# Kernel optimization log

Hardware: AMD Instinct MI355X
Metric: run time of the kernel (lower is better)

## Reference

```python
import jax, jax.numpy as jnp
import numpy as np

# dims: batch N, queries Q, frames F, patches-per-frame L, heads H, head_dim D
N, Q, F, L, H, D = 32, 64, 16, 196, 12, 64
E = H * D          # embed_dim = 768
K = F * L          # kv length = 3136


def setup_inputs() -> dict:
    key = jax.random.key(0)
    kq, kk, kv, km, kw1, kw2 = jax.random.split(key, 6)
    q = jax.random.normal(kq, (N, Q, E), dtype=jnp.float32)
    k = jax.random.normal(kk, (N, K, H, D), dtype=jnp.float32)
    v = jax.random.normal(kv, (N, K, H, D), dtype=jnp.float32)
    # frame-padding mask; guarantee >=1 valid patch per frame so the
    # per-frame softmax never sees an all -inf group (NaN otherwise)
    m = jax.random.bernoulli(km, 0.9, (N, K))
    m = m.reshape(N, F, L).at[:, :, 0].set(True).reshape(N, K)
    W_in = jax.random.normal(kw1, (E, E), dtype=jnp.float32) * 0.02   # in_proj (n_act=1)
    W_out = jax.random.normal(kw2, (E, E), dtype=jnp.float32) * 0.02  # out_proj
    return {"q": q, "k": k, "v": v, "m": m, "W_in": W_in, "W_out": W_out}


def reference(q, k, v, m, W_in, W_out):
    n, nq, e = q.shape
    h, d = H, e // H
    # in_proj (no bias) then split into heads; n_act == 1 so qs has one element
    qs = (q @ W_in.T).reshape(n, nq, h, d)
    # scaled QK affinity: [n, Q, K, h]
    aff = jnp.einsum('nqhc,nkhc->nqkh', qs * (d ** -0.5), k)
    # frame mask broadcast over queries and heads
    aff = jnp.where(m[:, None, :, None], aff, -jnp.inf)
    kn = aff.shape[2]
    # grouped softmax over patches within each frame (dim=-2 of the view)
    aff = jax.nn.softmax(aff.reshape(n, nq, F, kn // F, h), axis=-2)
    aff = aff.reshape(n, nq, kn, h)
    # mix with v and output projection
    mix = jnp.einsum('nqlh,nlhc->nqhc', aff, v)
    out = mix.reshape(n, nq, e) @ W_out.T
    # second return: stacked flattened qs, shape [n, n_act=1, Q, E]
    qs_out = qs.reshape(n, nq, e)[:, None]
    return out, qs_out
```

## Files before the change

kernel.cpp:

```cpp
#include <hip/hip_runtime.h>
#include <hip/hip_bf16.h>
#include <cfloat>

#define N_B 32
#define QN 64
#define FN 16
#define LP 196
#define HN 12
#define DH 64
#define EE 768
#define KLEN 3136
#define FPB 2
#define KROWS 208
#define VST 256

typedef short s16x4 __attribute__((ext_vector_type(4)));
typedef __bf16 bf16x4 __attribute__((ext_vector_type(4)));
typedef __bf16 bf16x8 __attribute__((ext_vector_type(8)));
typedef float f32x4 __attribute__((ext_vector_type(4)));
typedef unsigned u32x2 __attribute__((ext_vector_type(2)));

__device__ __forceinline__ bf16x8 cvt8(f32x4 a, f32x4 b) {
    bf16x8 r;
    r[0] = (__bf16)a[0]; r[1] = (__bf16)a[1]; r[2] = (__bf16)a[2]; r[3] = (__bf16)a[3];
    r[4] = (__bf16)b[0]; r[5] = (__bf16)b[1]; r[6] = (__bf16)b[2]; r[7] = (__bf16)b[3];
    return r;
}
__device__ __forceinline__ unsigned short bfb(float x) {
    return __builtin_bit_cast(unsigned short, (__bf16)x);
}
__device__ __forceinline__ unsigned pkbf(float lo, float hi) {
    return (unsigned)bfb(lo) | ((unsigned)bfb(hi) << 16);
}

__device__ __forceinline__ f32x4 mfma16(s16x4 a, s16x4 b, f32x4 c) {
#if __has_builtin(__builtin_amdgcn_mfma_f32_16x16x16_bf16)
    return __builtin_amdgcn_mfma_f32_16x16x16_bf16(__builtin_bit_cast(bf16x4, a),
                                                   __builtin_bit_cast(bf16x4, b), c, 0, 0, 0);
#elif __has_builtin(__builtin_amdgcn_mfma_f32_16x16x16bf16_1k)
    return __builtin_amdgcn_mfma_f32_16x16x16bf16_1k(a, b, c, 0, 0, 0);
#else
    f32x4 d;
    asm volatile("v_mfma_f32_16x16x16_bf16 %0, %1, %2, %3"
                 : "=v"(d) : "v"(a), "v"(b), "v"(c));
    return d;
#endif
}

__global__ __launch_bounds__(256) void gemm_mfma(const float* __restrict__ A,
                                                 const float* __restrict__ W,
                                                 float* __restrict__ C) {
    __shared__ unsigned short As[64 * 72];
    __shared__ unsigned short Ws[48 * 72];
    const int t = threadIdx.x;
    const int w = t >> 6, lane = t & 63, lr = lane & 15, lg = lane >> 4;
    const int m0 = blockIdx.x * 64;
    const int n0 = blockIdx.y * 48;

    f32x4 acc[3];
#pragma unroll
    for (int ct = 0; ct < 3; ++ct) acc[ct] = (f32x4){0.f, 0.f, 0.f, 0.f};

    for (int k0 = 0; k0 < EE; k0 += 32) {
        {
            int row = t >> 2, cb = t & 3;
            const float* src = A + (size_t)(m0 + row) * EE + k0 + cb * 8;
            f32x4 a = *(const f32x4*)src, b = *(const f32x4*)(src + 4);
            *(bf16x8*)&As[row * 72 + cb * 8] = cvt8(a, b);
        }
        if (t < 192) {
            int row = t >> 2, cb = t & 3;
            const float* src = W + (size_t)(n0 + row) * EE + k0 + cb * 8;
            f32x4 a = *(const f32x4*)src, b = *(const f32x4*)(src + 4);
            *(bf16x8*)&Ws[row * 72 + cb * 8] = cvt8(a, b);
        }
        __syncthreads();
        bf16x8 a = *(const bf16x8*)&As[(w * 16 + lr) * 72 + lg * 8];
#pragma unroll
        for (int ct = 0; ct < 3; ++ct) {
            bf16x8 b = *(const bf16x8*)&Ws[(ct * 16 + lr) * 72 + lg * 8];
            acc[ct] = __builtin_amdgcn_mfma_f32_16x16x32_bf16(a, b, acc[ct], 0, 0, 0);
        }
        __syncthreads();
    }
#pragma unroll
    for (int ct = 0; ct < 3; ++ct)
#pragma unroll
        for (int r = 0; r < 4; ++r)
            C[(size_t)(m0 + w * 16 + lg * 4 + r) * EE + n0 + ct * 16 + lr] = acc[ct][r];
}

__global__ __launch_bounds__(256) void zero_f32(float* __restrict__ p, int n4) {
    int i = blockIdx.x * 256 + threadIdx.x;
    if (i < n4) ((float4*)p)[i] = make_float4(0.f, 0.f, 0.f, 0.f);
}

__global__ __launch_bounds__(256, 2) void attn_mfma(const float* __restrict__ qs_g,
                                                    const float* __restrict__ k_g,
                                                    const float* __restrict__ v_g,
                                                    const int* __restrict__ m_g,
                                                    float* __restrict__ mix_g) {
    const int h = blockIdx.x, fg = blockIdx.y, n = blockIdx.z;

    __shared__ __attribute__((aligned(16))) unsigned short KV_s[64 * VST];
    __shared__ __attribute__((aligned(16))) float bias_s[224];

    const int t = threadIdx.x;
    const int w = t >> 6, lane = t & 63, lr = lane & 15, lg = lane >> 4;

    bf16x8 qb0, qb1;
    {
        const float* qp = qs_g + ((size_t)n * QN + w * 16 + lr) * EE + h * DH + lg * 8;
        f32x4 a = *(const f32x4*)qp, b = *(const f32x4*)(qp + 4);
        f32x4 c = *(const f32x4*)(qp + 32), d = *(const f32x4*)(qp + 36);
#pragma unroll
        for (int i = 0; i < 4; ++i) { a[i] *= 0.125f; b[i] *= 0.125f; c[i] *= 0.125f; d[i] *= 0.125f; }
        qb0 = cvt8(a, b);
        qb1 = cvt8(c, d);
    }

    float mix[4][4];
#pragma unroll
    for (int dt = 0; dt < 4; ++dt)
#pragma unroll
        for (int r = 0; r < 4; ++r) mix[dt][r] = 0.f;

    for (int ff = 0; ff < FPB; ++ff) {
        const size_t kbase = (size_t)n * KLEN + (size_t)(fg * FPB + ff) * LP;

        __syncthreads();

#pragma unroll
        for (int u = 0; u < 7; ++u) {
            int unit = t + 256 * u;
            if (unit < KROWS * 8) {
                int p = unit >> 3, blk = unit & 7;
                f32x4 a = {0.f, 0.f, 0.f, 0.f}, b = {0.f, 0.f, 0.f, 0.f};
                if (p < LP) {
                    const float* src = k_g + ((kbase + p) * HN + h) * DH + blk * 8;
                    a = *(const f32x4*)src;
                    b = *(const f32x4*)(src + 4);
                }
                *(bf16x8*)&KV_s[p * 64 + ((blk ^ (p & 7)) << 3)] = cvt8(a, b);
            }
        }
        if (t < 224) {
            float bv = -1e30f;
            if (t < LP && m_g[kbase + t] != 0) bv = 0.f;
            bias_s[t] = bv;
        }
        __syncthreads();

        f32x4 sc[13];
        __builtin_amdgcn_s_setprio(1);
#pragma unroll
        for (int tl = 0; tl < 13; ++tl) {
            int row = tl * 16 + lr;
            bf16x8 a0 = *(const bf16x8*)&KV_s[row * 64 + ((lg ^ (lr & 7)) << 3)];
            bf16x8 a1 = *(const bf16x8*)&KV_s[row * 64 + (((4 + lg) ^ (lr & 7)) << 3)];
            f32x4 z = {0.f, 0.f, 0.f, 0.f};
            z = __builtin_amdgcn_mfma_f32_16x16x32_bf16(a0, qb0, z, 0, 0, 0);
            sc[tl] = __builtin_amdgcn_mfma_f32_16x16x32_bf16(a1, qb1, z, 0, 0, 0);
        }
        __builtin_amdgcn_s_setprio(0);

        f32x4 va[4], vb[4];
#pragma unroll
        for (int u = 0; u < 4; ++u) {
            int unit = t + 256 * u;
            int pp = unit >> 3, d4 = unit & 7;
            int p0 = pp * 2;
            va[u] = (f32x4){0.f, 0.f, 0.f, 0.f};
            vb[u] = (f32x4){0.f, 0.f, 0.f, 0.f};
            if (p0 < LP) {
                const float* vg = v_g + ((kbase + p0) * HN + h) * DH + d4 * 4;
                va[u] = *(const f32x4*)vg;
                if (p0 + 1 < LP) vb[u] = *(const f32x4*)(vg + (size_t)HN * DH);
            }
        }

        float mx = -FLT_MAX;
#pragma unroll
        for (int tl = 0; tl < 13; ++tl) {
            f32x4 bv = *(const f32x4*)&bias_s[tl * 16 + lg * 4];
#pragma unroll
            for (int r = 0; r < 4; ++r) {
                float sv = sc[tl][r] + bv[r];
                sc[tl][r] = sv;
                mx = fmaxf(mx, sv);
            }
        }
        mx = fmaxf(mx, __shfl_xor(mx, 16));
        mx = fmaxf(mx, __shfl_xor(mx, 32));
        float sum = 0.f;
#pragma unroll
        for (int tl = 0; tl < 13; ++tl) {
            float e0 = __expf(sc[tl][0] - mx);
            float e1 = __expf(sc[tl][1] - mx);
            float e2 = __expf(sc[tl][2] - mx);
            float e3 = __expf(sc[tl][3] - mx);
            sum += (e0 + e1) + (e2 + e3);
            sc[tl][0] = e0; sc[tl][1] = e1; sc[tl][2] = e2; sc[tl][3] = e3;
        }
        sum += __shfl_xor(sum, 16);
        sum += __shfl_xor(sum, 32);
        float inv = 1.0f / sum;
        unsigned pk[13][2];
#pragma unroll
        for (int tl = 0; tl < 13; ++tl) {
            pk[tl][0] = pkbf(sc[tl][0] * inv, sc[tl][1] * inv);
            pk[tl][1] = pkbf(sc[tl][2] * inv, sc[tl][3] * inv);
        }

        __syncthreads();

#pragma unroll
        for (int u = 0; u < 4; ++u) {
            int unit = t + 256 * u;
            int pp = unit >> 3, d4 = unit & 7;
            int p0 = pp * 2;
            if (p0 < KROWS) {
                int blk = p0 >> 3, sub = p0 & 7;
#pragma unroll
                for (int i = 0; i < 4; ++i) {
                    int row = d4 * 4 + i;
                    int g = (row + 2 * (row >> 2)) & 7;
                    *(unsigned*)&KV_s[row * VST + (((blk ^ g) << 3) | sub)] = pkbf(va[u][i], vb[u][i]);
                }
            }
        }
#pragma unroll
        for (int u = 0; u < 4; ++u) {
            int unit = t + 256 * u;
            int pp = unit >> 3, d4 = unit & 7;
            int p0 = pp * 2;
            va[u] = (f32x4){0.f, 0.f, 0.f, 0.f};
            vb[u] = (f32x4){0.f, 0.f, 0.f, 0.f};
            if (p0 < LP) {
                const float* vg = v_g + ((kbase + p0) * HN + h) * DH + (8 + d4) * 4;
                va[u] = *(const f32x4*)vg;
                if (p0 + 1 < LP) vb[u] = *(const f32x4*)(vg + (size_t)HN * DH);
            }
        }
        __syncthreads();

        __builtin_amdgcn_s_setprio(1);
#pragma unroll
        for (int dt = 0; dt < 2; ++dt) {
            int row = dt * 16 + lr;
            int g = (row + 2 * (row >> 2)) & 7;
            f32x4 acc = {mix[dt][0], mix[dt][1], mix[dt][2], mix[dt][3]};
#pragma unroll
            for (int kt = 0; kt < 13; ++kt) {
                int c0 = kt * 16 + lg * 4;
                s16x4 b = *(const s16x4*)&KV_s[row * VST + ((((c0 >> 3) ^ g) << 3) | (c0 & 7))];
                s16x4 a = __builtin_bit_cast(s16x4, (u32x2){pk[kt][0], pk[kt][1]});
                acc = mfma16(a, b, acc);
            }
#pragma unroll
            for (int r = 0; r < 4; ++r) mix[dt][r] = acc[r];
        }
        __builtin_amdgcn_s_setprio(0);

#pragma unroll
        for (int u = 0; u < 4; ++u) {
            int unit = t + 256 * u;
            int pp = unit >> 3, d4 = unit & 7;
            int p0 = pp * 2;
            if (p0 < KROWS) {
                int blk = p0 >> 3, sub = p0 & 7;
#pragma unroll
                for (int i = 0; i < 4; ++i) {
                    int row = 32 + d4 * 4 + i;
                    int g = (row + 2 * (row >> 2)) & 7;
                    *(unsigned*)&KV_s[row * VST + (((blk ^ g) << 3) | sub)] = pkbf(va[u][i], vb[u][i]);
                }
            }
        }
        __syncthreads();

        __builtin_amdgcn_s_setprio(1);
#pragma unroll
        for (int dt = 2; dt < 4; ++dt) {
            int row = dt * 16 + lr;
            int g = (row + 2 * (row >> 2)) & 7;
            f32x4 acc = {mix[dt][0], mix[dt][1], mix[dt][2], mix[dt][3]};
#pragma unroll
            for (int kt = 0; kt < 13; ++kt) {
                int c0 = kt * 16 + lg * 4;
                s16x4 b = *(const s16x4*)&KV_s[row * VST + ((((c0 >> 3) ^ g) << 3) | (c0 & 7))];
                s16x4 a = __builtin_bit_cast(s16x4, (u32x2){pk[kt][0], pk[kt][1]});
                acc = mfma16(a, b, acc);
            }
#pragma unroll
            for (int r = 0; r < 4; ++r) mix[dt][r] = acc[r];
        }
        __builtin_amdgcn_s_setprio(0);
    }

#pragma unroll
    for (int dt = 0; dt < 4; ++dt)
#pragma unroll
        for (int r = 0; r < 4; ++r)
            atomicAdd(mix_g + ((size_t)n * QN + w * 16 + lg * 4 + r) * EE + h * DH + dt * 16 + lr,
                      mix[dt][r]);
}

extern "C" void kernel_launch(void* const* d_in, const int* in_sizes, int n_in,
                              void* d_out, int out_size, void* d_ws, size_t ws_size,
                              hipStream_t stream) {
    const float* q  = (const float*)d_in[0];
    const float* k  = (const float*)d_in[1];
    const float* v  = (const float*)d_in[2];
    const int*   m  = (const int*)d_in[3];
    const float* Wi = (const float*)d_in[4];
    const float* Wo = (const float*)d_in[5];

    float* out = (float*)d_out;
    float* qs  = out + (size_t)N_B * QN * EE;
    float* mix = (float*)d_ws;

    const int mix_n4 = (N_B * QN * EE) / 4;
    dim3 ggrid((N_B * QN) / 64, EE / 48);
    gemm_mfma<<<ggrid, 256, 0, stream>>>(q, Wi, qs);
    zero_f32<<<(mix_n4 + 255) / 256, 256, 0, stream>>>(mix, mix_n4);
    attn_mfma<<<dim3(HN, FN / FPB, N_B), 256, 0, stream>>>(qs, k, v, m, mix);
    gemm_mfma<<<ggrid, 256, 0, stream>>>(mix, Wo, out);
}
```

Measured before the change: 212.2 us.

## Prefetch next frame's K tile into registers and use LDS-only barriers

Loads the first frame's K tile and mask value into registers before the frame loop. Inside the loop it issues the global loads for the next frame's K during the V phase, so their latency overlaps the PV MFMAs. Two __syncthreads are replaced with a barrier that waits only on lgkmcnt, so outstanding global loads no longer stall at those barriers. The cost is many extra VGPRs (14 f32x4 plus 7 bf16x8), which may lower occupancy or cause spills.

```diff
diff --git a/kernel.cpp b/kernel.cpp
--- a/kernel.cpp
+++ b/kernel.cpp
@@ -31,6 +31,11 @@
 }
 __device__ __forceinline__ unsigned pkbf(float lo, float hi) {
     return (unsigned)bfb(lo) | ((unsigned)bfb(hi) << 16);
+}
+__device__ __forceinline__ void barrier_lds_only() {
+    asm volatile("s_waitcnt lgkmcnt(0)" ::: "memory");
+    __builtin_amdgcn_s_barrier();
+    __builtin_amdgcn_sched_barrier(0);
 }
 
 __device__ __forceinline__ f32x4 mfma16(s16x4 a, s16x4 b, f32x4 c) {
@@ -119,6 +124,25 @@
         qb1 = cvt8(c, d);
     }
 
+    bf16x8 kpre[7];
+    int mr;
+    {
+        const size_t kb0 = (size_t)n * KLEN + (size_t)(fg * FPB) * LP;
+#pragma unroll
+        for (int u = 0; u < 7; ++u) {
+            int unit = t + 256 * u;
+            int p = unit >> 3, blk = unit & 7;
+            f32x4 a = {0.f, 0.f, 0.f, 0.f}, b = {0.f, 0.f, 0.f, 0.f};
+            if (unit < KROWS * 8 && p < LP) {
+                const float* src = k_g + ((kb0 + p) * HN + h) * DH + blk * 8;
+                a = *(const f32x4*)src;
+                b = *(const f32x4*)(src + 4);
+            }
+            kpre[u] = cvt8(a, b);
+        }
+        mr = (t < LP) ? m_g[kb0 + t] : 0;
+    }
+
     float mix[4][4];
 #pragma unroll
     for (int dt = 0; dt < 4; ++dt)
@@ -135,20 +159,10 @@
             int unit = t + 256 * u;
             if (unit < KROWS * 8) {
                 int p = unit >> 3, blk = unit & 7;
-                f32x4 a = {0.f, 0.f, 0.f, 0.f}, b = {0.f, 0.f, 0.f, 0.f};
-                if (p < LP) {
-                    const float* src = k_g + ((kbase + p) * HN + h) * DH + blk * 8;
-                    a = *(const f32x4*)src;
-                    b = *(const f32x4*)(src + 4);
-                }
-                *(bf16x8*)&KV_s[p * 64 + ((blk ^ (p & 7)) << 3)] = cvt8(a, b);
-            }
-        }
-        if (t < 224) {
-            float bv = -1e30f;
-            if (t < LP && m_g[kbase + t] != 0) bv = 0.f;
-            bias_s[t] = bv;
-        }
+                *(bf16x8*)&KV_s[p * 64 + ((blk ^ (p & 7)) << 3)] = kpre[u];
+            }
+        }
+        if (t < 224) bias_s[t] = (t < LP && mr != 0) ? 0.f : -1e30f;
         __syncthreads();
 
         f32x4 sc[13];
@@ -242,7 +256,24 @@
                 if (p0 + 1 < LP) vb[u] = *(const f32x4*)(vg + (size_t)HN * DH);
             }
         }
-        __syncthreads();
+        f32x4 ka[7], kb[7];
+        if (ff + 1 < FPB) {
+            const size_t kbn = kbase + LP;
+#pragma unroll
+            for (int u = 0; u < 7; ++u) {
+                int unit = t + 256 * u;
+                int p = unit >> 3, blk = unit & 7;
+                ka[u] = (f32x4){0.f, 0.f, 0.f, 0.f};
+                kb[u] = (f32x4){0.f, 0.f, 0.f, 0.f};
+                if (unit < KROWS * 8 && p < LP) {
+                    const float* src = k_g + ((kbn + p) * HN + h) * DH + blk * 8;
+                    ka[u] = *(const f32x4*)src;
+                    kb[u] = *(const f32x4*)(src + 4);
+                }
+            }
+            mr = (t < LP) ? m_g[kbn + t] : 0;
+        }
+        barrier_lds_only();
 
         __builtin_amdgcn_s_setprio(1);
 #pragma unroll
@@ -277,7 +308,7 @@
                 }
             }
         }
-        __syncthreads();
+        barrier_lds_only();
 
         __builtin_amdgcn_s_setprio(1);
 #pragma unroll
@@ -296,6 +327,11 @@
             for (int r = 0; r < 4; ++r) mix[dt][r] = acc[r];
         }
         __builtin_amdgcn_s_setprio(0);
+
+        if (ff + 1 < FPB) {
+#pragma unroll
+            for (int u = 0; u < 7; ++u) kpre[u] = cvt8(ka[u], kb[u]);
+        }
     }
 
 #pragma unroll
```

New measurement: 251.0 us. 1.18x slower.
